# Optimization experiments

Measured on AMD Instinct MI355X. Metric: run time of the kernel, lower is better.

Reference implementation:

```python
import jax, jax.numpy as jnp
import numpy as np

N_QUBITS = 4

def _rx(theta):
    # RX(t) = [[cos t/2, -i sin t/2], [-i sin t/2, cos t/2]]; theta scalar or [B]
    c = jnp.cos(theta / 2).astype(jnp.complex64)
    s = (-1j * jnp.sin(theta / 2)).astype(jnp.complex64)
    return jnp.stack([jnp.stack([c, s], -1), jnp.stack([s, c], -1)], -2)

def _ry(theta):
    c = jnp.cos(theta / 2).astype(jnp.complex64)
    s = jnp.sin(theta / 2).astype(jnp.complex64)
    return jnp.stack([jnp.stack([c, -s], -1), jnp.stack([s, c], -1)], -2)

def _rz(theta):
    e0 = jnp.exp(-0.5j * theta).astype(jnp.complex64)
    e1 = jnp.exp(0.5j * theta).astype(jnp.complex64)
    z = jnp.zeros_like(e0)
    return jnp.stack([jnp.stack([e0, z], -1), jnp.stack([z, e1], -1)], -2)

def _apply_1q(psi, U, wire):
    # psi: [B,2,2,2,2]; U: [2,2] (shared) or [B,2,2] (per-batch angle)
    psi = jnp.moveaxis(psi, 1 + wire, -1)
    if U.ndim == 3:
        psi = jnp.einsum('bij,b...j->b...i', U, psi)
    else:
        psi = jnp.einsum('ij,b...j->b...i', U, psi)
    return jnp.moveaxis(psi, -1, 1 + wire)

def _cnot(psi, c, t):
    psi = jnp.moveaxis(psi, (1 + c, 1 + t), (-2, -1))
    psi = jnp.concatenate([psi[..., 0:1, :], psi[..., 1:2, ::-1]], axis=-2)
    return jnp.moveaxis(psi, (-2, -1), (1 + c, 1 + t))

def _measure_all_z(psi):
    p = psi.real ** 2 + psi.imag ** 2  # [B,2,2,2,2]
    outs = []
    for w in range(N_QUBITS):
        shape = [1] * (N_QUBITS + 1)
        shape[1 + w] = 2
        z = jnp.array([1.0, -1.0], dtype=p.dtype).reshape(shape)
        outs.append(jnp.sum(p * z, axis=tuple(range(1, N_QUBITS + 1))))
    return jnp.stack(outs, -1)  # [B,4]

def _qlayer(x, theta):
    # x: [B,4] encoding angles; theta: [4] trainable RX angles
    B = x.shape[0]
    psi = jnp.zeros((B, 2 ** N_QUBITS), jnp.complex64).at[:, 0].set(1.0)
    psi = psi.reshape((B,) + (2,) * N_QUBITS)
    # encoder: rx(w0), ry(w1), rz(w2), rx(w3)
    psi = _apply_1q(psi, _rx(x[:, 0]), 0)
    psi = _apply_1q(psi, _ry(x[:, 1]), 1)
    psi = _apply_1q(psi, _rz(x[:, 2]), 2)
    psi = _apply_1q(psi, _rx(x[:, 3]), 3)
    # trainable RX on each wire
    for w in range(N_QUBITS):
        psi = _apply_1q(psi, _rx(theta[w]), w)
    # CNOT ring 0->1,1->2,2->3,3->0
    for w in range(N_QUBITS):
        psi = _cnot(psi, w, (w + 1) % N_QUBITS)
    return _measure_all_z(psi)

def setup_inputs() -> dict:
    key = jax.random.key(0)
    ks = jax.random.split(key, 13)
    T, B, D, H, Q = 128, 2048, 128, 4, 4
    s = 1.0 / np.sqrt(D + H)
    inp = {
        'inputs': jax.random.normal(ks[0], (T, B, D), jnp.float32),
        'Wf': jax.random.uniform(ks[1], (Q, D + H), jnp.float32, -s, s),
        'bf': jax.random.uniform(ks[2], (Q,), jnp.float32, -s, s),
        'Wi': jax.random.uniform(ks[3], (Q, D + H), jnp.float32, -s, s),
        'bi': jax.random.uniform(ks[4], (Q,), jnp.float32, -s, s),
        'Wu': jax.random.uniform(ks[5], (Q, D + H), jnp.float32, -s, s),
        'bu': jax.random.uniform(ks[6], (Q,), jnp.float32, -s, s),
        'Wo': jax.random.uniform(ks[7], (Q, D + H), jnp.float32, -s, s),
        'bo': jax.random.uniform(ks[8], (Q,), jnp.float32, -s, s),
        'theta_f': jax.random.uniform(ks[9], (Q,), jnp.float32, 0.0, 2 * np.pi),
        'theta_i': jax.random.uniform(ks[10], (Q,), jnp.float32, 0.0, 2 * np.pi),
        'theta_u': jax.random.uniform(ks[11], (Q,), jnp.float32, 0.0, 2 * np.pi),
        'theta_o': jax.random.uniform(ks[12], (Q,), jnp.float32, 0.0, 2 * np.pi),
    }
    return inp

def reference(inputs, Wf, bf, Wi, bi, Wu, bu, Wo, bo, theta_f, theta_i, theta_u, theta_o):
    T, B, D = inputs.shape
    H = N_QUBITS  # hidden_dim == n_qubits (required by elementwise gate math)
    h0 = jnp.zeros((B, H), inputs.dtype)
    c0 = jnp.zeros((B, H), inputs.dtype)

    def step(carry, x):
        hx, cx = carry
        comb = jnp.concatenate([x, hx], axis=1)  # [B, D+H]
        f = jax.nn.sigmoid(_qlayer(comb @ Wf.T + bf, theta_f))
        i = jax.nn.sigmoid(_qlayer(comb @ Wi.T + bi, theta_i))
        g = jnp.tanh(_qlayer(comb @ Wu.T + bu, theta_u))
        o = jax.nn.sigmoid(_qlayer(comb @ Wo.T + bo, theta_o))
        cx = f * cx + i * g
        hx = o * jnp.tanh(cx)
        return (hx, cx), hx

    (hx, cx), stacked = jax.lax.scan(step, (h0, c0), inputs)
    return stacked, hx, cx
```

## Files before the change

kernel.cpp:

```cpp
#include <hip/hip_runtime.h>
#include <stdint.h>

__device__ __forceinline__ float fast_exp(float x) {
  return __builtin_amdgcn_exp2f(x * 1.4426950408889634f);
}
__device__ __forceinline__ float fast_rcp(float x) {
  return __builtin_amdgcn_rcpf(x);
}
__device__ __forceinline__ float fast_cos(float x) {
  return __builtin_amdgcn_cosf(__builtin_amdgcn_fractf(x * 0.15915494309189535f));
}
__device__ __forceinline__ float fast_sigmoid(float x) {
  return fast_rcp(1.0f + fast_exp(-x));
}
__device__ __forceinline__ float fast_tanh(float x) {
  return 1.0f - 2.0f * fast_rcp(1.0f + fast_exp(2.0f * x));
}
__device__ __forceinline__ float sigmoid_poly(float x) {
  float x2 = x * x;
  float p = fmaf(fmaf(fmaf(-2.1085373e-4f, x2, 2.0833334e-3f), x2,
                      -2.0833334e-2f), x2, 0.25f);
  return fmaf(x, p, 0.5f);
}
__device__ __forceinline__ float tanh_pade(float x) {
  float x2 = x * x;
  float num = x * fmaf(x2 + 105.f, x2, 945.f);
  float den = fmaf(fmaf(15.f, x2, 420.f), x2, 945.f);
  return num * fast_rcp(den);
}

template <int CTRL>
__device__ __forceinline__ float dppf(float v) {
  return __int_as_float(__builtin_amdgcn_update_dpp(
      0, __float_as_int(v), CTRL, 0xf, 0xf, true));
}
#define QP_XOR1 0xB1
#define QP_XOR2 0x4E
#define QP_XOR3 0x1B

__device__ __forceinline__ void gload_lds16(const float* gp, const float* lp) {
  __builtin_amdgcn_global_load_lds(
      reinterpret_cast<const uint32_t __attribute__((address_space(1)))*>(
          reinterpret_cast<uintptr_t>(gp)),
      reinterpret_cast<uint32_t __attribute__((address_space(3)))*>(
          reinterpret_cast<uintptr_t>(lp)),
      16, 0, 0);
}

__global__ __launch_bounds__(64) void qlstm_gemm(
    const float* __restrict__ x,
    const float* __restrict__ Wf, const float* __restrict__ bf,
    const float* __restrict__ Wi, const float* __restrict__ bi,
    const float* __restrict__ Wu, const float* __restrict__ bu,
    const float* __restrict__ Wo, const float* __restrict__ bo,
    const float* __restrict__ thf, const float* __restrict__ thi,
    const float* __restrict__ thu, const float* __restrict__ tho,
    float* __restrict__ Z, long long rows, int B, int D)
{
  __shared__ float buf[2][64][32];
  const long long base = (long long)blockIdx.x * 64;
  const int tid = threadIdx.x;
  const long long r = base + tid;
  const bool valid = r < rows;
  const int ldw = D + 4;
  const float* Ws[4] = {Wf, Wi, Wu, Wo};
  const float* bs[4] = {bf, bi, bu, bo};
  const float* ts[4] = {thf, thi, thu, tho};

  const int lgrp = tid >> 3;
  const int lcol = tid & 7;
  const int scol4 = lcol ^ lgrp;

  float acc[12];
#pragma unroll
  for (int g = 0; g < 4; ++g) {
    acc[g * 3 + 0] = bs[g][0] + ts[g][0];
    acc[g * 3 + 1] = bs[g][1];
    acc[g * 3 + 2] = bs[g][3] + ts[g][3];
  }

  const int nkc = D >> 5;

  auto issue = [&](int kc, int w) {
#pragma unroll
    for (int i = 0; i < 8; ++i) {
      long long gr = base + i * 8 + lgrp;
      if (gr >= rows) gr = rows - 1;
      const float* gp = x + gr * (long long)D + kc * 32 + scol4 * 4;
      gload_lds16(gp, &buf[w][i * 8][0]);
    }
  };

  issue(0, 0);
  if (nkc > 1) issue(1, 1);

  for (int kc = 0; kc < nkc; ++kc) {
    if (kc + 2 < nkc) {
      asm volatile("s_waitcnt vmcnt(8)" ::: "memory");
    } else {
      asm volatile("s_waitcnt vmcnt(0)" ::: "memory");
    }
    if (valid) {
      const float(*tb)[32] = buf[kc & 1];
#pragma unroll
      for (int k4 = 0; k4 < 8; ++k4) {
        float4 xv = *(const float4*)&tb[tid][(k4 ^ lcol) * 4];
        int k = k4 * 4;
#pragma unroll
        for (int g = 0; g < 4; ++g) {
#pragma unroll
          for (int jj = 0; jj < 3; ++jj) {
            int row2 = (jj == 2) ? 3 : jj;
            const float* wp = Ws[g] + row2 * ldw + kc * 32 + k;
            acc[g * 3 + jj] += xv.x * wp[0] + xv.y * wp[1] + xv.z * wp[2] + xv.w * wp[3];
          }
        }
      }
    }
    if (kc + 2 < nkc) issue(kc + 2, kc & 1);
  }

  if (valid) {
    long long t = r / B;
    int b = (int)(r - t * B);
    float4 s0 = make_float4(acc[0], acc[3], acc[6], acc[9]);
    float4 s1 = make_float4(acc[1], acc[4], acc[7], acc[10]);
    float4 s2 = make_float4(acc[2], acc[5], acc[8], acc[11]);
    *(float4*)(Z + ((t * 3 + 0) * (long long)B + b) * 4) = s0;
    *(float4*)(Z + ((t * 3 + 1) * (long long)B + b) * 4) = s1;
    *(float4*)(Z + ((t * 3 + 2) * (long long)B + b) * 4) = s2;
  }
}

__global__ __launch_bounds__(64) void qlstm_scan4(
    const float* __restrict__ Z,
    const float* __restrict__ Wf, const float* __restrict__ Wi,
    const float* __restrict__ Wu, const float* __restrict__ Wo,
    const float* __restrict__ thf, const float* __restrict__ thi,
    const float* __restrict__ thu, const float* __restrict__ tho,
    float* __restrict__ out, int T, int B, int D)
{
  const int gid = blockIdx.x * 64 + threadIdx.x;
  const int b = gid >> 2, q = gid & 3;
  if (b >= B) return;

  const float* Wg = (q == 0) ? Wf : (q == 1) ? Wi : (q == 2) ? Wu : Wo;
  const float* th = (q == 0) ? thf : (q == 1) ? thi : (q == 2) ? thu : tho;
  const int ldw = D + 4;
  const float ct1 = fast_cos(th[1]);
  const float m2c = fast_cos(th[2]);

  float wh[3][4];
#pragma unroll
  for (int jj = 0; jj < 3; ++jj) {
    int row = (jj == 2) ? 3 : jj;
#pragma unroll
    for (int d = 0; d < 4; ++d)
      wh[jj][d] = Wg[row * ldw + D + (q ^ d)];
  }
  const bool e0 = ((q & 1) == 0);
  const bool e1 = ((q & 2) == 0);

  float h = 0.f, c = 0.f;

  const float* Zg = Z + gid;
  const size_t tstr = (size_t)12 * B;
  const size_t pstr = (size_t)4 * B;
  float* hx  = out + (size_t)T * B * 4;
  float* cxp = hx + (size_t)B * 4;

  auto ld3 = [&](int t, float& z0, float& z1, float& z2) {
    const float* p = Zg + (size_t)t * tstr;
    z0 = p[0]; z1 = p[pstr]; z2 = p[2 * pstr];
  };

  auto step = [&](float z0, float z1, float z2, int t) {
    float h1 = dppf<QP_XOR1>(h);
    float h2 = dppf<QP_XOR2>(h);
    float h3 = dppf<QP_XOR3>(h);
    float a0 = fmaf(wh[0][0], h, fmaf(wh[0][1], h1, fmaf(wh[0][2], h2, fmaf(wh[0][3], h3, z0))));
    float a1 = fmaf(wh[1][0], h, fmaf(wh[1][1], h1, fmaf(wh[1][2], h2, fmaf(wh[1][3], h3, z1))));
    float a2 = fmaf(wh[2][0], h, fmaf(wh[2][1], h1, fmaf(wh[2][2], h2, fmaf(wh[2][3], h3, z2))));
    float m0 = fast_cos(a0);
    float m1 = ct1 * fast_cos(a1);
    float m3 = fast_cos(a2);
    float m01 = m0 * m1, m23 = m2c * m3;
    float g0 = m1 * m23;
    float g1 = m01;
    float g2 = m01 * m2c;
    float g3 = m01 * m23;
    float x0 = dppf<QP_XOR1>(g0);
    float x1 = dppf<QP_XOR1>(g1);
    float x2 = dppf<QP_XOR1>(g2);
    float x3 = dppf<QP_XOR1>(g3);
    float s0 = e0 ? g0 : x1;
    float s1 = e0 ? x0 : g1;
    float s2 = e0 ? g2 : x3;
    float s3 = e0 ? x2 : g3;
    float y0 = dppf<QP_XOR2>(s0);
    float y1 = dppf<QP_XOR2>(s1);
    float y2 = dppf<QP_XOR2>(s2);
    float y3 = dppf<QP_XOR2>(s3);
    float wf_ = e1 ? s0 : y2;
    float wi_ = e1 ? s1 : y3;
    float wu_ = e1 ? y0 : s2;
    float wo_ = e1 ? y1 : s3;
    float fg = sigmoid_poly(wf_);
    float ig = sigmoid_poly(wi_);
    float ug = tanh_pade(wu_);
    float og = sigmoid_poly(wo_);
    c = fmaf(fg, c, ig * ug);
    h = og * tanh_pade(c);
    out[(size_t)t * pstr + gid] = h;
  };

  float A0, A1, A2, B0, B1, B2, C0, C1, C2, D0, D1, D2;
  float E0, E1, E2, F0, F1, F2, G0, G1, G2, H0, H1, H2;
  if (T > 0) ld3(0, A0, A1, A2);
  if (T > 1) ld3(1, B0, B1, B2);
  if (T > 2) ld3(2, C0, C1, C2);
  if (T > 3) ld3(3, D0, D1, D2);
  if (T > 4) ld3(4, E0, E1, E2);
  if (T > 5) ld3(5, F0, F1, F2);
  if (T > 6) ld3(6, G0, G1, G2);
  if (T > 7) ld3(7, H0, H1, H2);

  int T8 = T & ~7;
  for (int t = 0; t < T8; t += 8) {
    { float z0 = A0, z1 = A1, z2 = A2;
      if (t + 8 < T) ld3(t + 8, A0, A1, A2);
      step(z0, z1, z2, t); }
    { float z0 = B0, z1 = B1, z2 = B2;
      if (t + 9 < T) ld3(t + 9, B0, B1, B2);
      step(z0, z1, z2, t + 1); }
    { float z0 = C0, z1 = C1, z2 = C2;
      if (t + 10 < T) ld3(t + 10, C0, C1, C2);
      step(z0, z1, z2, t + 2); }
    { float z0 = D0, z1 = D1, z2 = D2;
      if (t + 11 < T) ld3(t + 11, D0, D1, D2);
      step(z0, z1, z2, t + 3); }
    { float z0 = E0, z1 = E1, z2 = E2;
      if (t + 12 < T) ld3(t + 12, E0, E1, E2);
      step(z0, z1, z2, t + 4); }
    { float z0 = F0, z1 = F1, z2 = F2;
      if (t + 13 < T) ld3(t + 13, F0, F1, F2);
      step(z0, z1, z2, t + 5); }
    { float z0 = G0, z1 = G1, z2 = G2;
      if (t + 14 < T) ld3(t + 14, G0, G1, G2);
      step(z0, z1, z2, t + 6); }
    { float z0 = H0, z1 = H1, z2 = H2;
      if (t + 15 < T) ld3(t + 15, H0, H1, H2);
      step(z0, z1, z2, t + 7); }
  }
  for (int t = T8; t < T; ++t) {
    float z0, z1, z2;
    ld3(t, z0, z1, z2);
    step(z0, z1, z2, t);
  }
  hx[gid]  = h;
  cxp[gid] = c;
}

struct GK {
  float wh[4][3][4];
  float ct1[4];
  float m2c[4];
};

__device__ __forceinline__ void load_gk(GK& K,
    const float* Wf, const float* Wi, const float* Wu, const float* Wo,
    const float* thf, const float* thi, const float* thu, const float* tho,
    int D)
{
  const float* Ws[4] = {Wf, Wi, Wu, Wo};
  const float* ts[4] = {thf, thi, thu, tho};
  const int ldw = D + 4;
#pragma unroll
  for (int g = 0; g < 4; ++g) {
#pragma unroll
    for (int jj = 0; jj < 3; ++jj) {
      int row = (jj == 2) ? 3 : jj;
#pragma unroll
      for (int qq = 0; qq < 4; ++qq)
        K.wh[g][jj][qq] = Ws[g][row * ldw + D + qq];
    }
    K.ct1[g] = fast_cos(ts[g][1]);
    K.m2c[g] = fast_cos(ts[g][2]);
  }
}

__device__ __forceinline__ void qlstm_step_sc(const float a[12], const GK& K,
                                              float h[4], float c[4])
{
  float gv[4][4];
#pragma unroll
  for (int g = 0; g < 4; ++g) {
    float m0 = fast_cos(a[g * 3 + 0]);
    float m1 = K.ct1[g] * fast_cos(a[g * 3 + 1]);
    float m3 = fast_cos(a[g * 3 + 2]);
    float m01 = m0 * m1;
    float m23 = K.m2c[g] * m3;
    gv[g][0] = m1 * m23;
    gv[g][1] = m01;
    gv[g][2] = m01 * K.m2c[g];
    gv[g][3] = m01 * m23;
  }
#pragma unroll
  for (int qq = 0; qq < 4; ++qq) {
    float fg = fast_sigmoid(gv[0][qq]);
    float ig = fast_sigmoid(gv[1][qq]);
    float ug = fast_tanh(gv[2][qq]);
    float og = fast_sigmoid(gv[3][qq]);
    c[qq] = fg * c[qq] + ig * ug;
    h[qq] = og * fast_tanh(c[qq]);
  }
}

__global__ __launch_bounds__(256) void qlstm_fused(
    const float* __restrict__ x,
    const float* __restrict__ Wf, const float* __restrict__ bf,
    const float* __restrict__ Wi, const float* __restrict__ bi,
    const float* __restrict__ Wu, const float* __restrict__ bu,
    const float* __restrict__ Wo, const float* __restrict__ bo,
    const float* __restrict__ thf, const float* __restrict__ thi,
    const float* __restrict__ thu, const float* __restrict__ tho,
    float* __restrict__ out, int T, int B, int D)
{
  int b = blockIdx.x * 256 + threadIdx.x;
  if (b >= B) return;
  GK K;
  load_gk(K, Wf, Wi, Wu, Wo, thf, thi, thu, tho, D);
  const float* Ws[4] = {Wf, Wi, Wu, Wo};
  const float* bs[4] = {bf, bi, bu, bo};
  const float* ts[4] = {thf, thi, thu, tho};
  const int ldw = D + 4;

  float base[12];
#pragma unroll
  for (int g = 0; g < 4; ++g) {
    base[g * 3 + 0] = bs[g][0] + ts[g][0];
    base[g * 3 + 1] = bs[g][1];
    base[g * 3 + 2] = bs[g][3] + ts[g][3];
  }

  float h[4] = {0.f, 0.f, 0.f, 0.f};
  float c[4] = {0.f, 0.f, 0.f, 0.f};
  float* hx  = out + (size_t)T * B * 4;
  float* cxp = hx + (size_t)B * 4;

  for (int t = 0; t < T; ++t) {
    float a[12];
#pragma unroll
    for (int j = 0; j < 12; ++j) a[j] = base[j];
    const float* xp = x + ((size_t)t * B + b) * D;
    for (int k = 0; k < D; k += 4) {
      float4 xv = *(const float4*)(xp + k);
#pragma unroll
      for (int g = 0; g < 4; ++g) {
        const float* W = Ws[g];
#pragma unroll
        for (int jj = 0; jj < 3; ++jj) {
          int row = (jj == 2) ? 3 : jj;
          const float* wp = W + row * ldw + k;
          a[g * 3 + jj] += xv.x * wp[0] + xv.y * wp[1] + xv.z * wp[2] + xv.w * wp[3];
        }
      }
    }
#pragma unroll
    for (int g = 0; g < 4; ++g) {
#pragma unroll
      for (int jj = 0; jj < 3; ++jj) {
        a[g * 3 + jj] += K.wh[g][jj][0] * h[0] + K.wh[g][jj][1] * h[1]
                       + K.wh[g][jj][2] * h[2] + K.wh[g][jj][3] * h[3];
      }
    }
    qlstm_step_sc(a, K, h, c);
    *(float4*)(out + ((size_t)t * B + b) * 4) = make_float4(h[0], h[1], h[2], h[3]);
  }
  *(float4*)(hx + (size_t)b * 4)  = make_float4(h[0], h[1], h[2], h[3]);
  *(float4*)(cxp + (size_t)b * 4) = make_float4(c[0], c[1], c[2], c[3]);
}

extern "C" void kernel_launch(void* const* d_in, const int* in_sizes, int n_in,
                              void* d_out, int out_size, void* d_ws, size_t ws_size,
                              hipStream_t stream)
{
  const float* x   = (const float*)d_in[0];
  const float* Wf  = (const float*)d_in[1];
  const float* bf  = (const float*)d_in[2];
  const float* Wi  = (const float*)d_in[3];
  const float* bi  = (const float*)d_in[4];
  const float* Wu  = (const float*)d_in[5];
  const float* bu  = (const float*)d_in[6];
  const float* Wo  = (const float*)d_in[7];
  const float* bo  = (const float*)d_in[8];
  const float* thf = (const float*)d_in[9];
  const float* thi = (const float*)d_in[10];
  const float* thu = (const float*)d_in[11];
  const float* tho = (const float*)d_in[12];

  int DH = in_sizes[1] / 4;
  int D  = DH - 4;
  long long TB = (long long)in_sizes[0] / D;
  int B = (int)(((long long)out_size - 4 * TB) / 8);
  int T = (int)(TB / B);

  size_t zbytes = (size_t)TB * 12 * sizeof(float);
  if (ws_size >= zbytes && (D & 31) == 0) {
    float* Z = (float*)d_ws;
    int gblocks = (int)((TB + 63) / 64);
    qlstm_gemm<<<gblocks, 64, 0, stream>>>(x, Wf, bf, Wi, bi, Wu, bu, Wo, bo,
                                           thf, thi, thu, tho, Z, TB, B, D);
    int sthreads = B * 4;
    qlstm_scan4<<<(sthreads + 63) / 64, 64, 0, stream>>>(Z, Wf, Wi, Wu, Wo,
                                                         thf, thi, thu, tho,
                                                         (float*)d_out, T, B, D);
  } else {
    qlstm_fused<<<(B + 255) / 256, 256, 0, stream>>>(x, Wf, bf, Wi, bi, Wu, bu, Wo, bo,
                                                     thf, thi, thu, tho,
                                                     (float*)d_out, T, B, D);
  }
}
```

Measured before the change: 80.50 us.

## Replace async LDS double-buffering with synchronous tile loads and packed FMAs

The projection GEMM drops its double-buffered direct-to-LDS async loads with swizzled layout. Each chunk is now loaded synchronously through registers into a padded LDS tile, with barriers around the compute. The inner product uses v_pk_fma_f32 on paired accumulators, with weights read as float4 and passed in scalar registers. This halves the FMA instruction count, but it loses the load/compute overlap, and the 's' constraint requires the weight loads to be uniform.

```diff
diff --git a/kernel.cpp b/kernel.cpp
--- a/kernel.cpp
+++ b/kernel.cpp
@@ -1,5 +1,7 @@
 #include <hip/hip_runtime.h>
 #include <stdint.h>
+
+using f32x2 = __attribute__((ext_vector_type(2))) float;
 
 __device__ __forceinline__ float fast_exp(float x) {
   return __builtin_amdgcn_exp2f(x * 1.4426950408889634f);
@@ -38,13 +40,8 @@
 #define QP_XOR2 0x4E
 #define QP_XOR3 0x1B
 
-__device__ __forceinline__ void gload_lds16(const float* gp, const float* lp) {
-  __builtin_amdgcn_global_load_lds(
-      reinterpret_cast<const uint32_t __attribute__((address_space(1)))*>(
-          reinterpret_cast<uintptr_t>(gp)),
-      reinterpret_cast<uint32_t __attribute__((address_space(3)))*>(
-          reinterpret_cast<uintptr_t>(lp)),
-      16, 0, 0);
+__device__ __forceinline__ void pk_fma(f32x2& acc, f32x2 x, f32x2 w) {
+  asm("v_pk_fma_f32 %0, %1, %2, %0" : "+v"(acc) : "v"(x), "s"(w));
 }
 
 __global__ __launch_bounds__(64) void qlstm_gemm(
@@ -57,7 +54,7 @@
     const float* __restrict__ thu, const float* __restrict__ tho,
     float* __restrict__ Z, long long rows, int B, int D)
 {
-  __shared__ float buf[2][64][32];
+  __shared__ float tile[64][36];
   const long long base = (long long)blockIdx.x * 64;
   const int tid = threadIdx.x;
   const long long r = base + tid;
@@ -67,65 +64,57 @@
   const float* bs[4] = {bf, bi, bu, bo};
   const float* ts[4] = {thf, thi, thu, tho};
 
-  const int lgrp = tid >> 3;
-  const int lcol = tid & 7;
-  const int scol4 = lcol ^ lgrp;
-
-  float acc[12];
+  f32x2 acc[12];
 #pragma unroll
   for (int g = 0; g < 4; ++g) {
-    acc[g * 3 + 0] = bs[g][0] + ts[g][0];
-    acc[g * 3 + 1] = bs[g][1];
-    acc[g * 3 + 2] = bs[g][3] + ts[g][3];
+    acc[g * 3 + 0] = f32x2{bs[g][0] + ts[g][0], 0.f};
+    acc[g * 3 + 1] = f32x2{bs[g][1], 0.f};
+    acc[g * 3 + 2] = f32x2{bs[g][3] + ts[g][3], 0.f};
   }
 
   const int nkc = D >> 5;
-
-  auto issue = [&](int kc, int w) {
+  for (int kc = 0; kc < nkc; ++kc) {
 #pragma unroll
     for (int i = 0; i < 8; ++i) {
-      long long gr = base + i * 8 + lgrp;
-      if (gr >= rows) gr = rows - 1;
-      const float* gp = x + gr * (long long)D + kc * 32 + scol4 * 4;
-      gload_lds16(gp, &buf[w][i * 8][0]);
+      int f = i * 64 + tid;
+      int row = f >> 3, col = (f & 7) * 4;
+      long long gr = base + row;
+      if (gr < rows) {
+        float4 v = *(const float4*)(x + gr * (long long)D + kc * 32 + col);
+        *(float4*)&tile[row][col] = v;
+      }
     }
-  };
-
-  issue(0, 0);
-  if (nkc > 1) issue(1, 1);
-
-  for (int kc = 0; kc < nkc; ++kc) {
-    if (kc + 2 < nkc) {
-      asm volatile("s_waitcnt vmcnt(8)" ::: "memory");
-    } else {
-      asm volatile("s_waitcnt vmcnt(0)" ::: "memory");
-    }
+    __syncthreads();
     if (valid) {
-      const float(*tb)[32] = buf[kc & 1];
 #pragma unroll
       for (int k4 = 0; k4 < 8; ++k4) {
-        float4 xv = *(const float4*)&tb[tid][(k4 ^ lcol) * 4];
-        int k = k4 * 4;
+        float4 xv = *(float4*)&tile[tid][k4 * 4];
+        f32x2 xlo = {xv.x, xv.y}, xhi = {xv.z, xv.w};
 #pragma unroll
         for (int g = 0; g < 4; ++g) {
 #pragma unroll
           for (int jj = 0; jj < 3; ++jj) {
             int row2 = (jj == 2) ? 3 : jj;
-            const float* wp = Ws[g] + row2 * ldw + kc * 32 + k;
-            acc[g * 3 + jj] += xv.x * wp[0] + xv.y * wp[1] + xv.z * wp[2] + xv.w * wp[3];
+            const float* wp = Ws[g] + row2 * ldw + kc * 32 + k4 * 4;
+            float4 wv = *(const float4*)wp;
+            pk_fma(acc[g * 3 + jj], xlo, f32x2{wv.x, wv.y});
+            pk_fma(acc[g * 3 + jj], xhi, f32x2{wv.z, wv.w});
           }
         }
       }
     }
-    if (kc + 2 < nkc) issue(kc + 2, kc & 1);
+    __syncthreads();
   }
 
   if (valid) {
+    float a[12];
+#pragma unroll
+    for (int j = 0; j < 12; ++j) a[j] = acc[j].x + acc[j].y;
     long long t = r / B;
     int b = (int)(r - t * B);
-    float4 s0 = make_float4(acc[0], acc[3], acc[6], acc[9]);
-    float4 s1 = make_float4(acc[1], acc[4], acc[7], acc[10]);
-    float4 s2 = make_float4(acc[2], acc[5], acc[8], acc[11]);
+    float4 s0 = make_float4(a[0], a[3], a[6], a[9]);
+    float4 s1 = make_float4(a[1], a[4], a[7], a[10]);
+    float4 s2 = make_float4(a[2], a[5], a[8], a[11]);
     *(float4*)(Z + ((t * 3 + 0) * (long long)B + b) * 4) = s0;
     *(float4*)(Z + ((t * 3 + 1) * (long long)B + b) * 4) = s1;
     *(float4*)(Z + ((t * 3 + 2) * (long long)B + b) * 4) = s2;
```

New measurement: 71.98 us. -10.6%, faster.
